# Performance work log

Hardware: AMD Instinct MI355X
Metric: run time of the kernel (lower is better)

Reference implementation:

```python
import jax, jax.numpy as jnp
import numpy as np

N, IN_DIM, OUT_DIM, HEADS = 8192, 256, 64, 2

def setup_inputs() -> dict:
    key = jax.random.key(0)
    k1, k2, k3, k4, k5 = jax.random.split(key, 5)
    x = jax.random.normal(k1, (N, IN_DIM), dtype=jnp.float32)
    adj = jax.random.randint(k2, (N, N), 0, 2, dtype=jnp.int32)
    # nn.Linear(in_dim, out_dim*heads, bias=False): weight [out_dim*heads, in_dim]
    W = jax.random.normal(k3, (OUT_DIM * HEADS, IN_DIM), dtype=jnp.float32) / np.sqrt(IN_DIM)
    attn_l = jax.random.normal(k4, (HEADS, OUT_DIM), dtype=jnp.float32)
    attn_r = jax.random.normal(k5, (HEADS, OUT_DIM), dtype=jnp.float32)
    return {"x": x, "adj": adj, "W": W, "attn_l": attn_l, "attn_r": attn_r}

def reference(x, adj, W, attn_l, attn_r):
    n = x.shape[0]
    h = (x @ W.T).reshape(n, HEADS, OUT_DIM)          # [N, H, D]
    el = jnp.einsum('nhd,hd->nh', h, attn_l)           # [N, H]
    er = jnp.einsum('nhd,hd->nh', h, attn_r)           # [N, H]
    e = el[:, None, :] + er[None, :, :]                # [N, N, H]
    e = jnp.where(adj[:, :, None] == 0, -jnp.inf, e)
    a = jax.nn.softmax(e, axis=1)                      # softmax over source nodes j
    out = jnp.einsum('ijh,jhd->ihd', a, h)             # [N, H, D]
    return out.reshape(n, HEADS * OUT_DIM)
```

## Files before the change

kernel.cpp:

```cpp
#include <hip/hip_runtime.h>
#include <cstdint>
#include <cstddef>

#define N_NODES 8192
#define IN_DIM  256
#define OUT_DIM 64
#define HEADS   2
#define FEAT    128
#define NTILES  9
#define ACC_STRIDE 132
#define KSPLIT  8
#define PACK_BLOCKS 2048

typedef __bf16 bf16x8 __attribute__((ext_vector_type(8)));
typedef float  f32x4  __attribute__((ext_vector_type(4)));
typedef int    i32x4  __attribute__((ext_vector_type(4)));
typedef unsigned uu32x4 __attribute__((ext_vector_type(4)));

static __device__ __forceinline__ unsigned short f2bf(float f) {
  unsigned u = __float_as_uint(f);
  u += 0x7FFFu + ((u >> 16) & 1u);
  return (unsigned short)(u >> 16);
}

__global__ __launch_bounds__(256) void k_prep_pack(const float* __restrict__ x,
                                                   const float* __restrict__ W,
                                                   const float* __restrict__ attn_r,
                                                   const int* __restrict__ adj,
                                                   uint4* __restrict__ frag,
                                                   unsigned* __restrict__ bm) {
  __shared__ float xs[32][68];
  __shared__ float wl[128][68];
  __shared__ unsigned short pk[32][146];

  const int tid = threadIdx.x;

  if (blockIdx.x < PACK_BLOCKS) {
#pragma unroll
    for (int rr = 0; rr < 4; ++rr) {
      const int row = blockIdx.x * 4 + rr;
      const i32x4* p = (const i32x4*)(adj + (size_t)row * N_NODES) + tid * 8;
      unsigned w = 0;
#pragma unroll
      for (int i = 0; i < 8; ++i) {
        i32x4 v = __builtin_nontemporal_load(p + i);
        w |= (v[0] != 0 ? 1u : 0u) << (i*4 + 0);
        w |= (v[1] != 0 ? 1u : 0u) << (i*4 + 1);
        w |= (v[2] != 0 ? 1u : 0u) << (i*4 + 2);
        w |= (v[3] != 0 ? 1u : 0u) << (i*4 + 3);
      }
      bm[(size_t)row * 256 + tid] = w;
    }
    return;
  }

  const int kb = blockIdx.x - PACK_BLOCKS;
  const int tx = tid & 15, ty = tid >> 4;
  const int j0 = kb * 32;

  float acc[2][8] = {};

  for (int kc = 0; kc < IN_DIM; kc += 64) {
    __syncthreads();
#pragma unroll
    for (int p = 0; p < 2; p++) {
      const int slot = p*256 + tid;
      const int r = slot >> 4, k4 = slot & 15;
      *(float4*)&xs[r][k4*4] = *(const float4*)(x + (size_t)(j0 + r)*IN_DIM + kc + k4*4);
    }
#pragma unroll
    for (int p = 0; p < 8; p++) {
      const int slot = p*256 + tid;
      const int r = slot >> 4, k4 = slot & 15;
      *(float4*)&wl[r][k4*4] = *(const float4*)(W + (size_t)r*IN_DIM + kc + k4*4);
    }
    __syncthreads();
#pragma unroll
    for (int k4 = 0; k4 < 16; k4++) {
      float4 xr[2], wr[8];
#pragma unroll
      for (int i = 0; i < 2; i++) xr[i] = *(const float4*)&xs[ty + i*16][k4*4];
#pragma unroll
      for (int jj = 0; jj < 8; jj++) wr[jj] = *(const float4*)&wl[tx + jj*16][k4*4];
#pragma unroll
      for (int i = 0; i < 2; i++)
#pragma unroll
        for (int jj = 0; jj < 8; jj++)
          acc[i][jj] += xr[i].x*wr[jj].x + xr[i].y*wr[jj].y +
                        xr[i].z*wr[jj].z + xr[i].w*wr[jj].w;
    }
  }

  float ar[8];
#pragma unroll
  for (int jj = 0; jj < 8; jj++)
    ar[jj] = attn_r[((jj >> 2)) * OUT_DIM + ((tx + jj*16) & 63)];
  float e0[2] = {}, e1[2] = {};
#pragma unroll
  for (int i = 0; i < 2; i++) {
#pragma unroll
    for (int jj = 0; jj < 4; jj++) e0[i] += acc[i][jj] * ar[jj];
#pragma unroll
    for (int jj = 4; jj < 8; jj++) e1[i] += acc[i][jj] * ar[jj];
  }
#pragma unroll
  for (int m = 1; m <= 8; m <<= 1) {
#pragma unroll
    for (int i = 0; i < 2; i++) {
      e0[i] += __shfl_xor(e0[i], m);
      e1[i] += __shfl_xor(e1[i], m);
    }
  }
  float w0[2], w1[2];
#pragma unroll
  for (int i = 0; i < 2; i++) { w0[i] = __expf(e0[i]); w1[i] = __expf(e1[i]); }

#pragma unroll
  for (int i = 0; i < 2; i++) {
    const int row = ty + i*16;
#pragma unroll
    for (int jj = 0; jj < 8; jj++)
      pk[row][tx + jj*16] = f2bf((jj < 4 ? w0[i] : w1[i]) * acc[i][jj]);
    pk[row][128 + tx] = (tx == 0) ? f2bf(w0[i]) : (tx == 1) ? f2bf(w1[i]) : 0;
  }
  __syncthreads();

#pragma unroll
  for (int t = 0; t < 3; t++) {
    const int wid = t*256 + tid;
    if (wid < 576) {
      const int l = wid & 63, n = wid >> 6;
      const int col = n*16 + (l & 15), jb = (l >> 4) * 8;
      uint4 o;
      o.x = (unsigned)pk[jb+0][col] | ((unsigned)pk[jb+1][col] << 16);
      o.y = (unsigned)pk[jb+2][col] | ((unsigned)pk[jb+3][col] << 16);
      o.z = (unsigned)pk[jb+4][col] | ((unsigned)pk[jb+5][col] << 16);
      o.w = (unsigned)pk[jb+6][col] | ((unsigned)pk[jb+7][col] << 16);
      frag[((size_t)kb*NTILES + n)*64 + l] = o;
    }
  }
}

__global__ __launch_bounds__(256, 2) void k_main(const unsigned* __restrict__ bm,
                                                 const uint4* __restrict__ fragB,
                                                 float* __restrict__ accum) {
  const int mb = blockIdx.x >> 3;
  const int ks = blockIdx.x & 7;
  const int tid = threadIdx.x;
  const int wave = tid >> 6, lane = tid & 63;
  const int m16 = lane & 15, quad = lane >> 4;

  const int row0 = mb*128 + wave*32 + m16;
  const i32x4* a0p = (const i32x4*)bm + (size_t)row0*64 + ks*8;
  const i32x4* a1p = a0p + (size_t)16*64;
  const uu32x4* bb = (const uu32x4*)fragB + (size_t)(ks*32)*NTILES*64 + lane;

  f32x4 acc0[NTILES], acc1[NTILES];
#pragma unroll
  for (int n = 0; n < NTILES; n++) {
    acc0[n] = (f32x4){0.f, 0.f, 0.f, 0.f};
    acc1[n] = (f32x4){0.f, 0.f, 0.f, 0.f};
  }

  uu32x4 bvA[NTILES], bvB[NTILES];

  auto unpack = [&](unsigned wbits) -> bf16x8 {
    const unsigned b = (wbits >> (quad * 8)) & 0xFFu;
    unsigned u0 = (b & 1u   ? 0x3F80u : 0u) | (b & 2u   ? 0x3F800000u : 0u);
    unsigned u1 = (b & 4u   ? 0x3F80u : 0u) | (b & 8u   ? 0x3F800000u : 0u);
    unsigned u2 = (b & 16u  ? 0x3F80u : 0u) | (b & 32u  ? 0x3F800000u : 0u);
    unsigned u3 = (b & 64u  ? 0x3F80u : 0u) | (b & 128u ? 0x3F800000u : 0u);
    uu32x4 u = {u0, u1, u2, u3};
    return __builtin_bit_cast(bf16x8, u);
  };

  i32x4 aC0 = a0p[0], aC1 = a1p[0];
#pragma unroll
  for (int t = 0; t < NTILES; t++) bvA[t] = bb[(size_t)t*64];

  for (int g = 0; g < 8; ++g) {
    i32x4 aN0 = a0p[g + 1];
    i32x4 aN1 = a1p[g + 1];
#pragma unroll
    for (int j = 0; j < 4; ++j) {
      const int kk = g*4 + j;
      const uu32x4* bp = bb + (size_t)(kk + 1)*NTILES*64;
      if ((j & 1) == 0) {
#pragma unroll
        for (int t = 0; t < NTILES; t++) bvB[t] = bp[(size_t)t*64];
      } else {
#pragma unroll
        for (int t = 0; t < NTILES; t++) bvA[t] = bp[(size_t)t*64];
      }
      bf16x8 af0 = unpack((unsigned)aC0[j]);
      bf16x8 af1 = unpack((unsigned)aC1[j]);
      const uu32x4* bv = ((j & 1) == 0) ? bvA : bvB;
#pragma unroll
      for (int n = 0; n < NTILES; n++) {
        bf16x8 bfr = __builtin_bit_cast(bf16x8, bv[n]);
        acc0[n] = __builtin_amdgcn_mfma_f32_16x16x32_bf16(af0, bfr, acc0[n], 0, 0, 0);
      }
#pragma unroll
      for (int n = 0; n < NTILES; n++) {
        bf16x8 bfr = __builtin_bit_cast(bf16x8, bv[n]);
        acc1[n] = __builtin_amdgcn_mfma_f32_16x16x32_bf16(af1, bfr, acc1[n], 0, 0, 0);
      }
    }
    aC0 = aN0; aC1 = aN1;
  }

  const int rb0 = mb*128 + wave*32 + quad*4;
  float* op = accum + (size_t)ks*N_NODES*ACC_STRIDE;
#pragma unroll
  for (int n = 0; n < NTILES; n++) {
    if (n == 8 && m16 >= HEADS) continue;
#pragma unroll
    for (int r = 0; r < 4; r++) {
      op[(size_t)(rb0 + r)*ACC_STRIDE + n*16 + m16]      = acc0[n][r];
      op[(size_t)(rb0 + 16 + r)*ACC_STRIDE + n*16 + m16] = acc1[n][r];
    }
  }
}

__global__ void k_div(const float* __restrict__ acc, float* __restrict__ out) {
  const int tid = threadIdx.x;
  const int r = tid >> 5, c4 = (tid & 31) << 2;
  const int i = blockIdx.x * 8 + r;
  const int h = c4 >> 6;
  f32x4 num = (f32x4){0.f, 0.f, 0.f, 0.f};
  float den = 0.f;
#pragma unroll
  for (int s = 0; s < KSPLIT; s++) {
    const float* p = acc + ((size_t)s*N_NODES + i)*ACC_STRIDE;
    num += *(const f32x4*)(p + c4);
    den += p[FEAT + h];
  }
  f32x4 o = num / (f32x4){den, den, den, den};
  *(f32x4*)(out + (size_t)i*FEAT + c4) = o;
}

extern "C" void kernel_launch(void* const* d_in, const int* in_sizes, int n_in,
                              void* d_out, int out_size, void* d_ws, size_t ws_size,
                              hipStream_t stream) {
  const float* x      = (const float*)d_in[0];
  const int*   adj    = (const int*)  d_in[1];
  const float* W      = (const float*)d_in[2];
  const float* attn_r = (const float*)d_in[4];

  char* ws = (char*)d_ws;
  uint4*    frag = (uint4*)(ws + 0);
  unsigned* bm   = (unsigned*)(ws + (4u << 20));
  float*    acc  = (float*)(ws + (16u << 20));
  float*    out  = (float*)d_out;

  hipLaunchKernelGGL(k_prep_pack, dim3(PACK_BLOCKS + 256), dim3(256), 0, stream,
                     x, W, attn_r, adj, frag, bm);
  hipLaunchKernelGGL(k_main, dim3(512),  dim3(256), 0, stream, bm, frag, acc);
  hipLaunchKernelGGL(k_div,  dim3(1024), dim3(256), 0, stream, acc, out);
}
```

Baseline: 488.5 us.

## Pack adjacency with wave ballots and split prep into separate kernels

Adjacency packing now has each wave read consecutive int4 chunks across lanes, so loads are fully coalesced, and build 64-bit masks with __ballot instead of having each thread walk 8 strided int4 loads. The resulting bit layout changes, so k_main's A-fragment unpack is rewritten to gather bits from four words at a per-quad shift. The projection/frag prep moves to its own kernel launch. This aims to speed up the bandwidth-bound 256 MB adjacency read, at the cost of an extra launch and somewhat more unpack ALU work in the main loop.

Result: faster. 413.4 us (-15.4%).

```diff
diff --git a/kernel.cpp b/kernel.cpp
--- a/kernel.cpp
+++ b/kernel.cpp
@@ -10,7 +10,6 @@
 #define NTILES  9
 #define ACC_STRIDE 132
 #define KSPLIT  8
-#define PACK_BLOCKS 2048
 
 typedef __bf16 bf16x8 __attribute__((ext_vector_type(8)));
 typedef float  f32x4  __attribute__((ext_vector_type(4)));
@@ -23,40 +22,44 @@
   return (unsigned short)(u >> 16);
 }
 
-__global__ __launch_bounds__(256) void k_prep_pack(const float* __restrict__ x,
-                                                   const float* __restrict__ W,
-                                                   const float* __restrict__ attn_r,
-                                                   const int* __restrict__ adj,
-                                                   uint4* __restrict__ frag,
-                                                   unsigned* __restrict__ bm) {
+__global__ __launch_bounds__(256) void k_pack(const int* __restrict__ adj,
+                                              unsigned long long* __restrict__ bm64) {
+  const int tid = threadIdx.x;
+  const int wv = tid >> 6, lane = tid & 63;
+  const int row = blockIdx.x * 4 + wv;
+  const i32x4* rp = (const i32x4*)(adj + (size_t)row * N_NODES) + lane;
+  unsigned long long* op = bm64 + (size_t)row * 128;
+
+  for (int c = 0; c < 32; c += 8) {
+    i32x4 v[8];
+#pragma unroll
+    for (int i = 0; i < 8; ++i)
+      v[i] = __builtin_nontemporal_load(rp + (size_t)(c + i) * 64);
+#pragma unroll
+    for (int i = 0; i < 8; ++i) {
+      unsigned long long m0 = __ballot(v[i][0] != 0);
+      unsigned long long m1 = __ballot(v[i][1] != 0);
+      unsigned long long m2 = __ballot(v[i][2] != 0);
+      unsigned long long m3 = __ballot(v[i][3] != 0);
+      unsigned long long mv = (lane == 0) ? m0 : (lane == 1) ? m1
+                            : (lane == 2) ? m2 : m3;
+      if (lane < 4) op[(c + i) * 4 + lane] = mv;
+    }
+  }
+}
+
+__global__ __launch_bounds__(256) void k_prep(const float* __restrict__ x,
+                                              const float* __restrict__ W,
+                                              const float* __restrict__ attn_r,
+                                              uint4* __restrict__ frag) {
+  const int kb = blockIdx.x;
+  const int tid = threadIdx.x;
+  const int tx = tid & 15, ty = tid >> 4;
+  const int j0 = kb * 32;
+
   __shared__ float xs[32][68];
   __shared__ float wl[128][68];
   __shared__ unsigned short pk[32][146];
-
-  const int tid = threadIdx.x;
-
-  if (blockIdx.x < PACK_BLOCKS) {
-#pragma unroll
-    for (int rr = 0; rr < 4; ++rr) {
-      const int row = blockIdx.x * 4 + rr;
-      const i32x4* p = (const i32x4*)(adj + (size_t)row * N_NODES) + tid * 8;
-      unsigned w = 0;
-#pragma unroll
-      for (int i = 0; i < 8; ++i) {
-        i32x4 v = __builtin_nontemporal_load(p + i);
-        w |= (v[0] != 0 ? 1u : 0u) << (i*4 + 0);
-        w |= (v[1] != 0 ? 1u : 0u) << (i*4 + 1);
-        w |= (v[2] != 0 ? 1u : 0u) << (i*4 + 2);
-        w |= (v[3] != 0 ? 1u : 0u) << (i*4 + 3);
-      }
-      bm[(size_t)row * 256 + tid] = w;
-    }
-    return;
-  }
-
-  const int kb = blockIdx.x - PACK_BLOCKS;
-  const int tx = tid & 15, ty = tid >> 4;
-  const int j0 = kb * 32;
 
   float acc[2][8] = {};
 
@@ -141,7 +144,7 @@
   }
 }
 
-__global__ __launch_bounds__(256, 2) void k_main(const unsigned* __restrict__ bm,
+__global__ __launch_bounds__(256, 2) void k_main(const unsigned long long* __restrict__ bm64,
                                                  const uint4* __restrict__ fragB,
                                                  float* __restrict__ accum) {
   const int mb = blockIdx.x >> 3;
@@ -149,10 +152,11 @@
   const int tid = threadIdx.x;
   const int wave = tid >> 6, lane = tid & 63;
   const int m16 = lane & 15, quad = lane >> 4;
+  const int q2 = quad * 2;
 
   const int row0 = mb*128 + wave*32 + m16;
-  const i32x4* a0p = (const i32x4*)bm + (size_t)row0*64 + ks*8;
-  const i32x4* a1p = a0p + (size_t)16*64;
+  const i32x4* a0p = (const i32x4*)((const char*)bm64 + (size_t)row0*1024 + ks*128);
+  const i32x4* a1p = a0p + 1024;
   const uu32x4* bb = (const uu32x4*)fragB + (size_t)(ks*32)*NTILES*64 + lane;
 
   f32x4 acc0[NTILES], acc1[NTILES];
@@ -164,26 +168,31 @@
 
   uu32x4 bvA[NTILES], bvB[NTILES];
 
-  auto unpack = [&](unsigned wbits) -> bf16x8 {
-    const unsigned b = (wbits >> (quad * 8)) & 0xFFu;
-    unsigned u0 = (b & 1u   ? 0x3F80u : 0u) | (b & 2u   ? 0x3F800000u : 0u);
-    unsigned u1 = (b & 4u   ? 0x3F80u : 0u) | (b & 8u   ? 0x3F800000u : 0u);
-    unsigned u2 = (b & 16u  ? 0x3F80u : 0u) | (b & 32u  ? 0x3F800000u : 0u);
-    unsigned u3 = (b & 64u  ? 0x3F80u : 0u) | (b & 128u ? 0x3F800000u : 0u);
+  auto unpack = [&](unsigned w0, unsigned w1, unsigned w2, unsigned w3,
+                    int s) -> bf16x8 {
+    const unsigned t0 = (w0 >> s) & 3u;
+    const unsigned t1 = (w1 >> s) & 3u;
+    const unsigned t2 = (w2 >> s) & 3u;
+    const unsigned t3 = (w3 >> s) & 3u;
+    unsigned u0 = (t0 & 1u ? 0x3F80u : 0u) | (t1 & 1u ? 0x3F800000u : 0u);
+    unsigned u1 = (t2 & 1u ? 0x3F80u : 0u) | (t3 & 1u ? 0x3F800000u : 0u);
+    unsigned u2 = (t0 & 2u ? 0x3F80u : 0u) | (t1 & 2u ? 0x3F800000u : 0u);
+    unsigned u3 = (t2 & 2u ? 0x3F80u : 0u) | (t3 & 2u ? 0x3F800000u : 0u);
     uu32x4 u = {u0, u1, u2, u3};
     return __builtin_bit_cast(bf16x8, u);
   };
 
-  i32x4 aC0 = a0p[0], aC1 = a1p[0];
+  i32x4 c0a = a0p[0], c0b = a0p[1];
+  i32x4 c1a = a1p[0], c1b = a1p[1];
 #pragma unroll
   for (int t = 0; t < NTILES; t++) bvA[t] = bb[(size_t)t*64];
 
-  for (int g = 0; g < 8; ++g) {
-    i32x4 aN0 = a0p[g + 1];
-    i32x4 aN1 = a1p[g + 1];
-#pragma unroll
-    for (int j = 0; j < 4; ++j) {
-      const int kk = g*4 + j;
+  for (int g = 0; g < 4; ++g) {
+    i32x4 n0a = a0p[(g + 1)*2],     n0b = a0p[(g + 1)*2 + 1];
+    i32x4 n1a = a1p[(g + 1)*2],     n1b = a1p[(g + 1)*2 + 1];
+#pragma unroll
+    for (int j = 0; j < 8; ++j) {
+      const int kk = g*8 + j;
       const uu32x4* bp = bb + (size_t)(kk + 1)*NTILES*64;
       if ((j & 1) == 0) {
 #pragma unroll
@@ -192,8 +201,19 @@
 #pragma unroll
         for (int t = 0; t < NTILES; t++) bvA[t] = bp[(size_t)t*64];
       }
-      bf16x8 af0 = unpack((unsigned)aC0[j]);
-      bf16x8 af1 = unpack((unsigned)aC1[j]);
+      const int s = (j & 3)*8 + q2;
+      bf16x8 af0, af1;
+      if (j < 4) {
+        af0 = unpack((unsigned)c0a[0], (unsigned)c0a[2],
+                     (unsigned)c0b[0], (unsigned)c0b[2], s);
+        af1 = unpack((unsigned)c1a[0], (unsigned)c1a[2],
+                     (unsigned)c1b[0], (unsigned)c1b[2], s);
+      } else {
+        af0 = unpack((unsigned)c0a[1], (unsigned)c0a[3],
+                     (unsigned)c0b[1], (unsigned)c0b[3], s);
+        af1 = unpack((unsigned)c1a[1], (unsigned)c1a[3],
+                     (unsigned)c1b[1], (unsigned)c1b[3], s);
+      }
       const uu32x4* bv = ((j & 1) == 0) ? bvA : bvB;
 #pragma unroll
       for (int n = 0; n < NTILES; n++) {
@@ -206,7 +226,7 @@
         acc1[n] = __builtin_amdgcn_mfma_f32_16x16x32_bf16(af1, bfr, acc1[n], 0, 0, 0);
       }
     }
-    aC0 = aN0; aC1 = aN1;
+    c0a = n0a; c0b = n0b; c1a = n1a; c1b = n1b;
   }
 
   const int rb0 = mb*128 + wave*32 + quad*4;
@@ -248,13 +268,13 @@
   const float* attn_r = (const float*)d_in[4];
 
   char* ws = (char*)d_ws;
-  uint4*    frag = (uint4*)(ws + 0);
-  unsigned* bm   = (unsigned*)(ws + (4u << 20));
-  float*    acc  = (float*)(ws + (16u << 20));
-  float*    out  = (float*)d_out;
-
-  hipLaunchKernelGGL(k_prep_pack, dim3(PACK_BLOCKS + 256), dim3(256), 0, stream,
-                     x, W, attn_r, adj, frag, bm);
-  hipLaunchKernelGGL(k_main, dim3(512),  dim3(256), 0, stream, bm, frag, acc);
+  uint4*              frag = (uint4*)(ws + 0);
+  unsigned long long* bm64 = (unsigned long long*)(ws + (4u << 20));
+  float*              acc  = (float*)(ws + (16u << 20));
+  float*              out  = (float*)d_out;
+
+  hipLaunchKernelGGL(k_pack, dim3(2048), dim3(256), 0, stream, adj, bm64);
+  hipLaunchKernelGGL(k_prep, dim3(256),  dim3(256), 0, stream, x, W, attn_r, frag);
+  hipLaunchKernelGGL(k_main, dim3(512),  dim3(256), 0, stream, bm64, frag, acc);
   hipLaunchKernelGGL(k_div,  dim3(1024), dim3(256), 0, stream, acc, out);
 }
```
